# Performance work log

Hardware: AMD Instinct MI355X
Metric: run time of the kernel (lower is better)

Reference implementation:

```python
import jax, jax.numpy as jnp
import numpy as np

SEQ_LEN, BATCH, HID, EMB, VOCAB, LAYERS = 64, 64, 512, 512, 10000, 2


def setup_inputs() -> dict:
    key = jax.random.key(0)
    ks = jax.random.split(key, 8)
    k = float(np.sqrt(1.0 / HID))
    u = lambda kk, shape: jax.random.uniform(kk, shape, jnp.float32, -k, k)
    return {
        "inputs": jax.random.randint(ks[0], (SEQ_LEN, BATCH), 0, VOCAB, dtype=jnp.int32),
        "hidden": jnp.zeros((LAYERS, BATCH, HID), jnp.float32),
        "emb_table": jax.random.uniform(ks[1], (VOCAB, EMB), jnp.float32, -0.1, 0.1),
        "Wx": u(ks[2], (LAYERS, EMB, 3 * HID)),
        "Uh": u(ks[3], (LAYERS, HID, 2 * HID)),
        "Uht": u(ks[4], (LAYERS, HID, HID)),
        "b_rzh": jnp.zeros((LAYERS, 3 * HID), jnp.float32),
        "dec_w": jax.random.uniform(ks[5], (VOCAB, HID), jnp.float32, -0.1, 0.1),
        "dec_b": jnp.zeros((VOCAB,), jnp.float32),
    }


def _gru_cell(x, h, Wx, Uh, Uht, b):
    # x: (B, E), h: (B, H)
    wx = x @ Wx + b                      # (B, 3H)
    uh = h @ Uh                          # (B, 2H)
    W_rx, W_zx, W_hx = jnp.split(wx, 3, axis=1)
    U_rh, U_zh = jnp.split(uh, 2, axis=1)
    r = jax.nn.sigmoid(W_rx + U_rh)
    z = jax.nn.sigmoid(W_zx + U_zh)
    h_tilde = jnp.tanh(W_hx + (r * h) @ Uht)
    return (1.0 - z) * h + z * h_tilde


def reference(inputs, hidden, emb_table, Wx, Uh, Uht, b_rzh, dec_w, dec_b):
    # inputs: (S, B) int; hidden: (L, B, H)
    embedded = emb_table[inputs]  # (S, B, E); dropout is identity (dp_keep_prob=1.0)

    def step(h_prev, x_t):
        inp = x_t
        new_h = []
        for l in range(LAYERS):
            hl = _gru_cell(inp, h_prev[l], Wx[l], Uh[l], Uht[l], b_rzh[l])
            new_h.append(hl)
            inp = hl
        logits_t = inp @ dec_w.T + dec_b  # (B, V)
        return jnp.stack(new_h), logits_t

    h_final, logits = jax.lax.scan(step, hidden, embedded)
    return logits, h_final  # (S, B, V), (L, B, H)
```

## Files before the change

### kernel.cpp

```cpp
#include <hip/hip_runtime.h>
#include <hip/hip_bf16.h>


#define SEQ 64
#define BPX 8

typedef short s16x8 __attribute__((ext_vector_type(8)));
typedef float f32x4 __attribute__((ext_vector_type(4)));
typedef int   i32x4 __attribute__((ext_vector_type(4)));
typedef unsigned long long ull;

static __device__ __forceinline__ unsigned short f2bf(float f){
    unsigned int u = __float_as_uint(f);
    return (unsigned short)((u + 0x7FFFu + ((u >> 16) & 1u)) >> 16);
}
static __device__ __forceinline__ float bf2f(unsigned short s){
    return __uint_as_float(((unsigned int)s) << 16);
}
static __device__ __forceinline__ float sigm(float x){
    return __fdividef(1.0f, 1.0f + __expf(-x));
}
static __device__ __forceinline__ float tanh_fast(float x){
    float ax = fabsf(x);
    float e = __expf(-2.0f * ax);
    float r = __fdividef(1.0f - e, 1.0f + e);
    return copysignf(r, x);
}
static __device__ __forceinline__ ull pack4bf(const float v[4]){
    union { ull u; unsigned short s[4]; } x;
    x.s[0]=f2bf(v[0]); x.s[1]=f2bf(v[1]); x.s[2]=f2bf(v[2]); x.s[3]=f2bf(v[3]);
    return x.u;
}
#define SC_LD16_NW(T,A) \
  asm volatile("global_load_dwordx4 %0, %1, off sc0 sc1" : "=&v"(T) : "v"(A) : "memory")
#define SC_WAIT() asm volatile("s_waitcnt vmcnt(0)" ::: "memory")
static __device__ __forceinline__ void sc_st8(void* p, ull v){
    asm volatile("global_store_dwordx2 %0, %1, off sc0 sc1" :: "v"(p), "v"(v) : "memory");
}

__global__ void prep_kernel(const int* __restrict__ inputs, const float* __restrict__ hidden,
    const float* __restrict__ emb, const float* __restrict__ Wx, const float* __restrict__ Uh,
    const float* __restrict__ Uht, const float* __restrict__ dec_w,
    unsigned short* __restrict__ emb_bf, unsigned short* __restrict__ WxT0,
    unsigned short* __restrict__ UhT0, unsigned short* __restrict__ UhtT0,
    unsigned short* __restrict__ Wx1T, unsigned short* __restrict__ Uh1T,
    unsigned short* __restrict__ UhtT1, unsigned short* __restrict__ decpad,
    float* __restrict__ HH, unsigned short* __restrict__ HHbf,
    unsigned short* __restrict__ H0m, unsigned int* __restrict__ barzone)
{
    const long long stride = (long long)gridDim.x * blockDim.x;
    const long long t0 = (long long)blockIdx.x * blockDim.x + threadIdx.x;
    for (long long i = t0; i < 4096LL*512; i += stride){
        int r = (int)(i >> 9), k = (int)(i & 511);
        emb_bf[i] = f2bf(emb[(long long)inputs[r]*512 + k]);
    }
    for (long long i = t0; i < 1536LL*512; i += stride){
        int n = (int)(i >> 9), k = (int)(i & 511);
        WxT0[i] = f2bf(Wx[(long long)k*1536 + n]);
    }
    for (long long i = t0; i < 1024LL*512; i += stride){
        int n = (int)(i >> 9), k = (int)(i & 511);
        UhT0[i] = f2bf(Uh[(long long)k*1024 + n]);
    }
    for (long long i = t0; i < 512LL*512; i += stride){
        int n = (int)(i >> 9), k = (int)(i & 511);
        UhtT0[i] = f2bf(Uht[(long long)k*512 + n]);
    }
    for (long long i = t0; i < 1536LL*512; i += stride){
        int n = (int)(i >> 9), k = (int)(i & 511);
        Wx1T[i] = f2bf(Wx[(long long)(512 + k)*1536 + n]);
    }
    for (long long i = t0; i < 1024LL*512; i += stride){
        int n = (int)(i >> 9), k = (int)(i & 511);
        Uh1T[i] = f2bf(Uh[(long long)(512 + k)*1024 + n]);
    }
    for (long long i = t0; i < 512LL*512; i += stride){
        int n = (int)(i >> 9), k = (int)(i & 511);
        UhtT1[i] = f2bf(Uht[(long long)(512 + k)*512 + n]);
    }
    for (long long i = t0; i < 10112LL*512; i += stride){
        int n = (int)(i >> 9), k = (int)(i & 511);
        decpad[i] = (n < 10000) ? f2bf(dec_w[(long long)n*512 + k]) : (unsigned short)0;
    }
    for (long long i = t0; i < 65536; i += stride){
        int b = (int)(i >> 10), c = (int)(i & 1023);
        int l = c >> 9, j = c & 511;
        float v = hidden[((long long)l*64 + b)*512 + j];
        HH[i] = v; HHbf[i] = f2bf(v);
    }
    for (long long i = t0; i < 32768; i += stride){
        int b = (int)(i >> 9), j = (int)(i & 511);
        H0m[i] = f2bf(hidden[(long long)b*512 + j]);
    }
    for (long long i = t0; i < 4096; i += stride) barzone[i] = 0u;
}

__global__ __launch_bounds__(256) void gemm128(const unsigned short* __restrict__ A,
    const unsigned short* __restrict__ BT, int M, int N, int K, int mode,
    float* __restrict__ outF, unsigned short* __restrict__ outB,
    const float* __restrict__ bias, int Nreal)
{
    __shared__ unsigned short Ash[128*32];
    __shared__ unsigned short Bsh[128*32];
    const int nT = N >> 7;
    const int mb = blockIdx.x / nT, nb = blockIdx.x % nT;
    const int tid = threadIdx.x;
    const int lane = tid & 63, wId = tid >> 6;
    const int wm = wId >> 1, wn = wId & 1;
    const int ln = lane & 15, kg = lane >> 4;
    f32x4 acc[4][4];
    #pragma unroll
    for (int mt = 0; mt < 4; ++mt)
        #pragma unroll
        for (int nt = 0; nt < 4; ++nt) acc[mt][nt] = f32x4{0.f,0.f,0.f,0.f};

    for (int kc = 0; kc < K; kc += 32){
        #pragma unroll
        for (int it = 0; it < 2; ++it){
            int flat = it*256 + tid;
            int row = flat >> 2, kq = flat & 3;
            *(int4*)(&Ash[flat*8]) = *(const int4*)(A + (long long)(mb*128 + row)*K + kc + kq*8);
            *(int4*)(&Bsh[flat*8]) = *(const int4*)(BT + (long long)(nb*128 + row)*K + kc + kq*8);
        }
        __syncthreads();
        s16x8 af[4], bfv[4];
        #pragma unroll
        for (int mt = 0; mt < 4; ++mt) af[mt]  = *(const s16x8*)(&Ash[(wm*64 + mt*16 + ln)*32 + kg*8]);
        #pragma unroll
        for (int nt = 0; nt < 4; ++nt) bfv[nt] = *(const s16x8*)(&Bsh[(wn*64 + nt*16 + ln)*32 + kg*8]);
        #pragma unroll
        for (int mt = 0; mt < 4; ++mt)
            #pragma unroll
            for (int nt = 0; nt < 4; ++nt)
                acc[mt][nt] = __builtin_amdgcn_mfma_f32_16x16x32_bf16(af[mt], bfv[nt], acc[mt][nt], 0, 0, 0);
        __syncthreads();
    }
    #pragma unroll
    for (int mt = 0; mt < 4; ++mt)
        #pragma unroll
        for (int nt = 0; nt < 4; ++nt)
            #pragma unroll
            for (int r = 0; r < 4; ++r){
                int row = mb*128 + wm*64 + mt*16 + kg*4 + r;
                int col = nb*128 + wn*64 + nt*16 + ln;
                float v = acc[mt][nt][r];
                if (mode == 0){
                    outB[(long long)row*N + col] = f2bf(v);
                } else {
                    if (col < Nreal) outF[(long long)row*Nreal + col] = v + bias[col];
                }
            }
}

static __device__ __forceinline__ void gsyncp(unsigned int* flags, int fidx, int pbase,
                                              unsigned gen){
    SC_WAIT();
    __syncthreads();
    if (threadIdx.x < 64){
        if (threadIdx.x == 0){
            asm volatile("global_store_dword %0, %1, off sc0 sc1"
                         :: "v"(flags + fidx*32), "v"(gen) : "memory");
        }
        const unsigned int* p = flags + (pbase + (threadIdx.x & 15))*32;
        unsigned v = gen; int it = 0;
        do {
            if (threadIdx.x < 16){
                asm volatile("global_load_dword %0, %1, off sc0 sc1\n\ts_waitcnt vmcnt(0)"
                             : "=v"(v) : "v"(p) : "memory");
            }
        } while (__ballot(v >= gen) != ~0ull && ++it < (1 << 20));
    }
    __syncthreads();
    asm volatile("buffer_inv" ::: "memory");
}

template<int KIT, int PITCH, int WSTRIDE>
static __device__ __forceinline__ f32x4 mmT16(const unsigned short* __restrict__ W,
    const char* __restrict__ lds, int ln, int kg, f32x4 acc)
{
    #pragma unroll 4
    for (int k = 0; k < KIT; ++k){
        s16x8 bv = *(const s16x8*)(lds + ((ln*PITCH + k*64 + kg*16) ^ ((ln & 7) << 4)));
        s16x8 av = *(const s16x8*)(W + ln*WSTRIDE + k*32 + kg*8);
        acc = __builtin_amdgcn_mfma_f32_16x16x32_bf16(av, bv, acc, 0, 0, 0);
    }
    return acc;
}

__global__ __launch_bounds__(512, 1) void gru_kernel(
    float* __restrict__ HHf, unsigned short* __restrict__ HHbf,
    const unsigned short* __restrict__ UhT0, const unsigned short* __restrict__ UhtT0,
    const unsigned short* __restrict__ Wx1T, const unsigned short* __restrict__ Uh1T,
    const unsigned short* __restrict__ UhtT1,
    const unsigned short* __restrict__ WX0,
    unsigned short* __restrict__ rh0, unsigned short* __restrict__ rh1,
    float* __restrict__ z0, float* __restrict__ z1, float* __restrict__ P3,
    unsigned short* __restrict__ H2bf, unsigned short* __restrict__ H0m,
    const float* __restrict__ b_rzh,
    float* __restrict__ outTail, unsigned int* __restrict__ barzone)
{
    __shared__ __align__(16) char smem[32768];
    __shared__ int s_xcc, s_lrank;
    const int tid = threadIdx.x, lane = tid & 63, wv = tid >> 6;
    const int ln = lane & 15, kg = lane >> 4;

    if (tid == 0){
        unsigned xcc;
        asm volatile("s_getreg_b32 %0, hwreg(HW_REG_XCC_ID)" : "=s"(xcc));
        xcc &= 7u;
        s_xcc = (int)xcc;
        s_lrank = (int)atomicAdd(barzone + 8 + xcc, 1u);
    }
    __syncthreads();
    const int lrank = s_lrank;
    if (lrank >= BPX) return;
    const int xcc = s_xcc;
    const int grp = xcc >> 1;
    const bool L0 = (xcc & 1) == 0;
    const int g16 = grp * 16;
    const int lw = lrank*8 + wv;
    const int fidx = xcc*8 + lrank;
    const int pbase = grp*16;
    unsigned int* flags = barzone + 256;
    const float* b0 = b_rzh;
    const float* b1 = b_rzh + 1536;
    const f32x4 zero = {0.f, 0.f, 0.f, 0.f};
    unsigned gen = 0;

    for (int ss = 0; ss <= SEQ; ++ss){
        if (L0){
            const int4* src = (const int4*)HHbf;
            int4 t[2];
            #pragma unroll
            for (int j = 0; j < 2; ++j){
                const int c = tid + j*512, row = c >> 6, col = c & 63;
                t[j] = src[(g16 + row)*128 + col];
            }
            #pragma unroll
            for (int j = 0; j < 2; ++j){
                const int c = tid + j*512, row = c >> 6, col = c & 63;
                *(int4*)(smem + ((row*1024 + col*16) ^ ((row & 7) << 4))) = t[j];
            }
        } else {
            i32x4 tm[2]; int4 tl[2];
            const char* srcm = (const char*)H0m;
            const int4* srch = (const int4*)HHbf;
            #pragma unroll
            for (int j = 0; j < 2; ++j){
                const int c = tid + j*512, row = c >> 6, col = c & 63;
                SC_LD16_NW(tm[j], srcm + ((long long)(g16 + row)*64 + col)*16);
                tl[j] = srch[(g16 + row)*128 + 64 + col];
            }
            SC_WAIT();
            #pragma unroll
            for (int j = 0; j < 2; ++j){
                const int c = tid + j*512, row = c >> 6, col = c & 63;
                *(i32x4*)(smem + ((row*2048 + col*16) ^ ((row & 7) << 4))) = tm[j];
                *(int4*)(smem + ((row*2048 + 1024 + col*16) ^ ((row & 7) << 4))) = tl[j];
            }
        }
        __syncthreads();
        if (L0){
            if (ss < SEQ){
                const int n0 = lw*16, nq = n0 + kg*4;
                const int b = g16 + ln;
                union { ull u; unsigned short s[4]; } wx;
                wx.u = *(const ull*)(WX0 + (long long)(ss*64 + b)*1536 + nq);
                f32x4 acc = mmT16<16,1024,512>(UhT0 + n0*512, smem, ln, kg, zero);
                f32x4 bias = *(const f32x4*)(b0 + nq);
                float sg[4];
                #pragma unroll
                for (int r = 0; r < 4; ++r)
                    sg[r] = sigm(acc[r] + bf2f(wx.s[r]) + bias[r]);
                if (nq < 512){
                    union { ull u; unsigned short s[4]; } h;
                    h.u = *(const ull*)(smem + ((ln*1024 + nq*2) ^ ((ln & 7) << 4)));
                    float rv[4];
                    #pragma unroll
                    for (int r = 0; r < 4; ++r) rv[r] = sg[r] * bf2f(h.s[r]);
                    *(ull*)(rh0 + b*512 + nq) = pack4bf(rv);
                } else {
                    f32x4 zz = {sg[0], sg[1], sg[2], sg[3]};
                    *(f32x4*)(z0 + b*512 + (nq - 512)) = zz;
                }
            }
        } else {
            if (ss >= 1){
                const int n0 = lw*16, nq = n0 + kg*4;
                const int b = g16 + ln;
                f32x4 acc = mmT16<16,2048,512>(Wx1T + n0*512, smem, ln, kg, zero);
                acc = mmT16<16,2048,512>(Uh1T + n0*512, smem + 1024, ln, kg, acc);
                f32x4 bias = *(const f32x4*)(b1 + nq);
                if (nq < 512){
                    union { ull u; unsigned short s[4]; } h;
                    h.u = *(const ull*)(smem + ((ln*2048 + 1024 + nq*2) ^ ((ln & 7) << 4)));
                    float rv[4];
                    #pragma unroll
                    for (int r = 0; r < 4; ++r)
                        rv[r] = sigm(acc[r] + bias[r]) * bf2f(h.s[r]);
                    *(ull*)(rh1 + b*512 + nq) = pack4bf(rv);
                } else {
                    float sg[4];
                    #pragma unroll
                    for (int r = 0; r < 4; ++r)
                        sg[r] = sigm(acc[r] + bias[r]);
                    f32x4 zz = {sg[0], sg[1], sg[2], sg[3]};
                    *(f32x4*)(z1 + b*512 + (nq - 512)) = zz;
                }
                if (lw < 32){
                    const int n0b = 1024 + lw*16, nqb = n0b + kg*4;
                    f32x4 acc2 = mmT16<16,2048,512>(Wx1T + (long long)n0b*512, smem, ln, kg, zero);
                    *(f32x4*)(P3 + b*512 + (nqb - 1024)) = acc2;
                }
            }
        }
        ++gen; gsyncp(flags, fidx, pbase, gen);

        {
            const int4* src = (const int4*)(L0 ? rh0 : rh1);
            int4 t[2];
            #pragma unroll
            for (int j = 0; j < 2; ++j){
                const int c = tid + j*512, row = c >> 6, col = c & 63;
                t[j] = src[(g16 + row)*64 + col];
            }
            #pragma unroll
            for (int j = 0; j < 2; ++j){
                const int c = tid + j*512, row = c >> 6, col = c & 63;
                *(int4*)(smem + ((row*1024 + col*16) ^ ((row & 7) << 4))) = t[j];
            }
        }
        __syncthreads();
        if (lw < 32){
            if (L0 && ss < SEQ){
                const int n0 = lw*16, nq = n0 + kg*4;
                const int b = g16 + ln;
                union { ull u; unsigned short s[4]; } wx;
                wx.u = *(const ull*)(WX0 + (long long)(ss*64 + b)*1536 + 1024 + nq);
                f32x4 zv  = *(const f32x4*)(z0 + b*512 + nq);
                f32x4 hpv = *(const f32x4*)(HHf + b*1024 + nq);
                f32x4 acc = mmT16<16,1024,512>(UhtT0 + n0*512, smem, ln, kg, zero);
                f32x4 bias = *(const f32x4*)(b0 + 1024 + nq);
                float hn[4];
                #pragma unroll
                for (int r = 0; r < 4; ++r){
                    float pre = acc[r] + bf2f(wx.s[r]) + bias[r];
                    float ht = tanh_fast(pre);
                    hn[r] = (1.0f - zv[r])*hpv[r] + zv[r]*ht;
                }
                f32x4 hv = {hn[0], hn[1], hn[2], hn[3]};
                *(f32x4*)(HHf + b*1024 + nq) = hv;
                ull pb = pack4bf(hn);
                *(ull*)(HHbf + b*1024 + nq) = pb;
                sc_st8(H0m + b*512 + nq, pb);
            } else if (!L0 && ss >= 1){
                const int t = ss - 1;
                const int n0 = lw*16, nq = n0 + kg*4;
                const int b = g16 + ln;
                f32x4 ppv = *(const f32x4*)(P3 + b*512 + nq);
                f32x4 zv  = *(const f32x4*)(z1 + b*512 + nq);
                f32x4 hpv = *(const f32x4*)(HHf + b*1024 + 512 + nq);
                f32x4 acc = mmT16<16,1024,512>(UhtT1 + n0*512, smem, ln, kg, zero);
                f32x4 bias = *(const f32x4*)(b1 + 1024 + nq);
                float hn[4];
                #pragma unroll
                for (int r = 0; r < 4; ++r){
                    float pre = acc[r] + ppv[r] + bias[r];
                    float ht = tanh_fast(pre);
                    hn[r] = (1.0f - zv[r])*hpv[r] + zv[r]*ht;
                }
                f32x4 hv = {hn[0], hn[1], hn[2], hn[3]};
                *(f32x4*)(HHf + b*1024 + 512 + nq) = hv;
                ull pb = pack4bf(hn);
                *(ull*)(HHbf + b*1024 + 512 + nq) = pb;
                *(ull*)(H2bf + (long long)(t*64 + b)*512 + nq) = pb;
            }
        }
        ++gen; gsyncp(flags, fidx, pbase, gen);
    }

    {
        const int l = L0 ? 0 : 1;
        const int c = lrank*512 + tid;
        if (c < 2048){
            const int b = g16 + (c >> 7), j4 = c & 127;
            f32x4 v = *(const f32x4*)(HHf + b*1024 + l*512 + j4*4);
            *(f32x4*)(outTail + l*32768 + b*512 + j4*4) = v;
        }
    }
}

extern "C" void kernel_launch(void* const* d_in, const int* in_sizes, int n_in,
                              void* d_out, int out_size, void* d_ws, size_t ws_size,
                              hipStream_t stream)
{
    const int*   inputs = (const int*)d_in[0];
    const float* hidden = (const float*)d_in[1];
    const float* emb    = (const float*)d_in[2];
    const float* Wx     = (const float*)d_in[3];
    const float* Uh     = (const float*)d_in[4];
    const float* Uht    = (const float*)d_in[5];
    const float* b_rzh  = (const float*)d_in[6];
    const float* dec_w  = (const float*)d_in[7];
    const float* dec_b  = (const float*)d_in[8];
    float* out = (float*)d_out;

    char* w = (char*)d_ws;
    size_t off = 0;
    auto alloc = [&](size_t bytes)->char*{
        char* p = w + off; off = (off + bytes + 255) & ~(size_t)255; return p;
    };
    unsigned short* emb_bf = (unsigned short*)alloc(4096LL*512*2);
    unsigned short* WxT0   = (unsigned short*)alloc(1536LL*512*2);
    unsigned short* WX0    = (unsigned short*)alloc(4096LL*1536*2);
    unsigned short* UhT0   = (unsigned short*)alloc(1024LL*512*2);
    unsigned short* UhtT0  = (unsigned short*)alloc(512LL*512*2);
    unsigned short* Wx1T   = (unsigned short*)alloc(1536LL*512*2);
    unsigned short* Uh1T   = (unsigned short*)alloc(1024LL*512*2);
    unsigned short* UhtT1  = (unsigned short*)alloc(512LL*512*2);
    unsigned short* decpad = (unsigned short*)alloc(10112LL*512*2);
    float*          HH     = (float*)alloc(65536*4);
    unsigned short* HHbf   = (unsigned short*)alloc(65536*2);
    unsigned short* H0m    = (unsigned short*)alloc(64*512*2);
    unsigned short* rh0    = (unsigned short*)alloc(64*512*2);
    unsigned short* rh1    = (unsigned short*)alloc(64*512*2);
    float*          z0     = (float*)alloc(64*512*4);
    float*          z1     = (float*)alloc(64*512*4);
    float*          P3     = (float*)alloc(64*512*4);
    unsigned short* H2bf   = (unsigned short*)alloc(4096LL*512*2);
    unsigned int*   barzone= (unsigned int*)alloc(16384);
    if (off > ws_size) return;

    prep_kernel<<<1024, 256, 0, stream>>>(inputs, hidden, emb, Wx, Uh, Uht, dec_w,
        emb_bf, WxT0, UhT0, UhtT0, Wx1T, Uh1T, UhtT1, decpad, HH, HHbf, H0m, barzone);

    gemm128<<<dim3(32*12), 256, 0, stream>>>(emb_bf, WxT0, 4096, 1536, 512,
        0, nullptr, WX0, nullptr, 1536);

    gru_kernel<<<dim3(256), 512, 0, stream>>>(HH, HHbf, UhT0, UhtT0, Wx1T, Uh1T,
        UhtT1, WX0, rh0, rh1, z0, z1, P3, H2bf, H0m, b_rzh, out + 40960000, barzone);

    gemm128<<<dim3(32*79), 256, 0, stream>>>(H2bf, decpad, 4096, 10112, 512,
        1, out, nullptr, dec_b, 10000);
}
```

Measured before the change: 1.421 ms.

## Decouple GRU layer XCC pairs with ring-buffered hidden state and one-way barriers

Each GRU barrier used to wait on all 16 blocks of both layers in an XCC pair. Now each barrier waits mainly on the 8 blocks in its own XCC. Layer 0 blocks only wait on layer 1 with a lag of a few generations, and layer 1 waits on layer 0 at its second barrier. The layer-0 hidden handoff buffer H0m becomes a 4-slot ring so layer 0 can run ahead without overwriting data layer 1 still reads. This cuts cross-XCC coupling on the per-step barrier, at the cost of more ring memory and subtle correctness conditions on the lag window.

```diff
diff --git a/kernel.cpp b/kernel.cpp
--- a/kernel.cpp
+++ b/kernel.cpp
@@ -88,8 +88,9 @@
         float v = hidden[((long long)l*64 + b)*512 + j];
         HH[i] = v; HHbf[i] = f2bf(v);
     }
-    for (long long i = t0; i < 32768; i += stride){
-        int b = (int)(i >> 9), j = (int)(i & 511);
+    for (long long i = t0; i < 4LL*32768; i += stride){
+        int idx = (int)(i & 32767);
+        int b = idx >> 9, j = idx & 511;
         H0m[i] = f2bf(hidden[(long long)b*512 + j]);
     }
     for (long long i = t0; i < 4096; i += stride) barzone[i] = 0u;
@@ -152,8 +153,8 @@
             }
 }
 
-static __device__ __forceinline__ void gsyncp(unsigned int* flags, int fidx, int pbase,
-                                              unsigned gen){
+static __device__ __forceinline__ void gsyncx(unsigned int* flags, int fidx, unsigned gen,
+                                              int ownBase, int otherBase, int otherGen){
     SC_WAIT();
     __syncthreads();
     if (threadIdx.x < 64){
@@ -161,14 +162,20 @@
             asm volatile("global_store_dword %0, %1, off sc0 sc1"
                          :: "v"(flags + fidx*32), "v"(gen) : "memory");
         }
-        const unsigned int* p = flags + (pbase + (threadIdx.x & 15))*32;
-        unsigned v = gen; int it = 0;
+        const int li = threadIdx.x;
+        const unsigned int* p = flags;
+        unsigned need = 0; bool active = false;
+        if (li < BPX){ p = flags + (ownBase + li)*32; need = gen; active = true; }
+        else if (li < 2*BPX && otherGen > 0){
+            p = flags + (otherBase + (li - BPX))*32; need = (unsigned)otherGen; active = true;
+        }
+        unsigned v = need; int it = 0;
         do {
-            if (threadIdx.x < 16){
+            if (active){
                 asm volatile("global_load_dword %0, %1, off sc0 sc1\n\ts_waitcnt vmcnt(0)"
                              : "=v"(v) : "v"(p) : "memory");
             }
-        } while (__ballot(v >= gen) != ~0ull && ++it < (1 << 20));
+        } while (__ballot(v >= need) != ~0ull && ++it < (1 << 20));
     }
     __syncthreads();
     asm volatile("buffer_inv" ::: "memory");
@@ -220,7 +227,7 @@
     const int g16 = grp * 16;
     const int lw = lrank*8 + wv;
     const int fidx = xcc*8 + lrank;
-    const int pbase = grp*16;
+    const int ownB = xcc*8, othB = (xcc ^ 1)*8;
     unsigned int* flags = barzone + 256;
     const float* b0 = b_rzh;
     const float* b1 = b_rzh + 1536;
@@ -243,7 +250,7 @@
             }
         } else {
             i32x4 tm[2]; int4 tl[2];
-            const char* srcm = (const char*)H0m;
+            const char* srcm = (const char*)(H0m + (long long)((ss + 3) & 3)*32768);
             const int4* srch = (const int4*)HHbf;
             #pragma unroll
             for (int j = 0; j < 2; ++j){
@@ -314,7 +321,9 @@
                 }
             }
         }
-        ++gen; gsyncp(flags, fidx, pbase, gen);
+        ++gen;
+        if (L0) gsyncx(flags, fidx, gen, ownB, othB, (int)gen - 6);
+        else    gsyncx(flags, fidx, gen, ownB, othB, 0);
 
         {
             const int4* src = (const int4*)(L0 ? rh0 : rh1);
@@ -352,7 +361,7 @@
                 *(f32x4*)(HHf + b*1024 + nq) = hv;
                 ull pb = pack4bf(hn);
                 *(ull*)(HHbf + b*1024 + nq) = pb;
-                sc_st8(H0m + b*512 + nq, pb);
+                sc_st8(H0m + (long long)(ss & 3)*32768 + b*512 + nq, pb);
             } else if (!L0 && ss >= 1){
                 const int t = ss - 1;
                 const int n0 = lw*16, nq = n0 + kg*4;
@@ -376,7 +385,9 @@
                 *(ull*)(H2bf + (long long)(t*64 + b)*512 + nq) = pb;
             }
         }
-        ++gen; gsyncp(flags, fidx, pbase, gen);
+        ++gen;
+        if (L0) gsyncx(flags, fidx, gen, ownB, othB, 0);
+        else    gsyncx(flags, fidx, gen, ownB, othB, (int)gen);
     }
 
     {
@@ -421,7 +432,7 @@
     unsigned short* decpad = (unsigned short*)alloc(10112LL*512*2);
     float*          HH     = (float*)alloc(65536*4);
     unsigned short* HHbf   = (unsigned short*)alloc(65536*2);
-    unsigned short* H0m    = (unsigned short*)alloc(64*512*2);
+    unsigned short* H0m    = (unsigned short*)alloc(4LL*32768*2);
     unsigned short* rh0    = (unsigned short*)alloc(64*512*2);
     unsigned short* rh1    = (unsigned short*)alloc(64*512*2);
     float*          z0     = (float*)alloc(64*512*4);
```

Result: faster. 1.370 ms (-3.6%).
